# Kernel tuning notes

Measured on AMD Instinct MI355X. Metric: run time of the kernel, lower is better.

## Reference

```python
import jax, jax.numpy as jnp
import numpy as np

HIDDEN = 100


def gcn_conv(x, W, b, src, dst, w, n):
    # GCNConv with symmetric normalization (self-loops already appended).
    xw = x @ W                                   # [N, H]
    deg = jax.ops.segment_sum(w, dst, num_segments=n)
    dinv = jnp.where(deg > 0, jax.lax.rsqrt(deg), 0.0)
    norm = dinv[src] * w * dinv[dst]             # [E]
    agg = jax.ops.segment_sum(norm[:, None] * xw[src], dst, num_segments=n)
    return agg + b


def setup_inputs() -> dict:
    key = jax.random.key(0)
    ks = jax.random.split(key, 16)
    N, F, E, H = 100000, 128, 1600000, HIDDEN
    x = jax.random.normal(ks[0], (N, F), dtype=jnp.float32)
    edge_index = jax.random.randint(ks[1], (2, E), 0, N, dtype=jnp.int64)
    edge_weight = jax.random.uniform(ks[2], (E,), dtype=jnp.float32)
    sF = 1.0 / np.sqrt(F)
    sH2 = 1.0 / np.sqrt(2 * H)
    sH = 1.0 / np.sqrt(H)
    inp = {
        "x": x, "edge_index": edge_index, "edge_weight": edge_weight,
        "Wcz": jax.random.normal(ks[3], (F, H), jnp.float32) * sF,
        "bcz": jnp.zeros((H,), jnp.float32),
        "Wcr": jax.random.normal(ks[4], (F, H), jnp.float32) * sF,
        "bcr": jnp.zeros((H,), jnp.float32),
        "Wch": jax.random.normal(ks[5], (F, H), jnp.float32) * sF,
        "bch": jnp.zeros((H,), jnp.float32),
        "Wlz": jax.random.normal(ks[6], (2 * H, H), jnp.float32) * sH2,
        "blz": jnp.zeros((H,), jnp.float32),
        "Wlr": jax.random.normal(ks[7], (2 * H, H), jnp.float32) * sH2,
        "blr": jnp.zeros((H,), jnp.float32),
        "Wlh": jax.random.normal(ks[8], (2 * H, H), jnp.float32) * sH2,
        "blh": jnp.zeros((H,), jnp.float32),
        "Wout": jax.random.normal(ks[9], (H, 1), jnp.float32) * sH,
        "bout": jnp.zeros((1,), jnp.float32),
    }
    return inp


def reference(x, edge_index, edge_weight,
              Wcz, bcz, Wcr, bcr, Wch, bch,
              Wlz, blz, Wlr, blr, Wlh, blh,
              Wout, bout):
    N = x.shape[0]
    # add self-loops with weight 1 (GCNConv default)
    loop = jnp.arange(N, dtype=edge_index.dtype)
    src = jnp.concatenate([edge_index[0], loop])
    dst = jnp.concatenate([edge_index[1], loop])
    w = jnp.concatenate([edge_weight, jnp.ones((N,), edge_weight.dtype)])

    H0 = jnp.zeros((N, HIDDEN), x.dtype)  # TGCN initial hidden state

    cz = gcn_conv(x, Wcz, bcz, src, dst, w, N)
    Z = jax.nn.sigmoid(jnp.concatenate([cz, H0], axis=1) @ Wlz + blz)

    cr = gcn_conv(x, Wcr, bcr, src, dst, w, N)
    R = jax.nn.sigmoid(jnp.concatenate([cr, H0], axis=1) @ Wlr + blr)

    ch = gcn_conv(x, Wch, bch, src, dst, w, N)
    Ht = jnp.tanh(jnp.concatenate([ch, H0 * R], axis=1) @ Wlh + blh)

    Hn = Z * H0 + (1.0 - Z) * Ht
    h = jax.nn.relu(Hn)
    return h @ Wout + bout
```

## Files before the change

### kernel.cpp

```cpp
#include <hip/hip_runtime.h>

#define FEAT 128
#define HID  100
#define CHUNK 2048

typedef __attribute__((ext_vector_type(8))) short short8;
typedef __attribute__((ext_vector_type(4))) float f32x4;

__device__ __forceinline__ unsigned short f2bf(float f) {
    union { float f; unsigned int u; } v; v.f = f;
    unsigned int r = v.u + 0x7fffu + ((v.u >> 16) & 1u);
    return (unsigned short)(r >> 16);
}

__device__ __forceinline__ int get_edge(const void* ei, int f64, long long pos) {
    return f64 ? (int)((const long long*)ei)[pos] : ((const int*)ei)[pos];
}

__device__ __forceinline__ int detect_f64(const void* ei) {
    const int* p = (const int*)ei;
    unsigned long long b = __ballot(p[2 * (threadIdx.x & 63) + 1] == 0);
    return b == ~0ull;
}

__device__ __forceinline__ void scan_buckets(const int* __restrict__ bucketCnt,
                                             int NB, int* bs) {
    int t = threadIdx.x;
    int v = (t < NB) ? bucketCnt[t] : 0;
    if (t < NB) bs[t] = v;
    __syncthreads();
    for (int off = 1; off < NB; off <<= 1) {
        int tv = (t < NB && t >= off) ? bs[t - off] : 0;
        __syncthreads();
        if (t < NB) bs[t] += tv;
        __syncthreads();
    }
    int incl = (t < NB) ? bs[t] : 0;
    __syncthreads();
    if (t < NB) bs[t] = incl - v;
    if (t == NB - 1) bs[NB] = incl;
    __syncthreads();
}

__global__ __launch_bounds__(256)
void k_front(const float* __restrict__ Wcz, const float* __restrict__ bcz,
             const float* __restrict__ Wch, const float* __restrict__ bch,
             const float* __restrict__ Wlz, const float* __restrict__ blz,
             const float* __restrict__ Wlh, const float* __restrict__ blh,
             const float* __restrict__ Wout,
             unsigned short* __restrict__ WB, float* __restrict__ bfold_ext,
             float* __restrict__ WoutZ,
             const void* ei, int* __restrict__ bucketCnt,
             int* __restrict__ blockBase, int NB, int E) {
    const int FOLDB = 130;
    __shared__ int hist[1024];
    if (blockIdx.x < FOLDB) {
        int idx = blockIdx.x * 256 + threadIdx.x;
        if (idx < FEAT * 256) {
            int k = idx >> 8, n = idx & 255;
            float val = 0.f;
            if (n < HID) {
                for (int m = 0; m < HID; m++) val += Wcz[k * HID + m] * Wlz[m * HID + n];
            } else if (n >= 128 && n < 128 + HID) {
                int c = n - 128;
                for (int m = 0; m < HID; m++) val += Wch[k * HID + m] * Wlh[m * HID + c];
            }
            int ni = n >> 4, lc = n & 15, ks = k >> 5, hi = (k >> 3) & 3, j = k & 7;
            WB[(((ni * 4 + ks) * 64 + hi * 16 + lc) << 3) + j] = f2bf(val);
        } else if (idx < FEAT * 256 + 256) {
            int c = idx - FEAT * 256;
            float v = 0.f;
            if (c < HID) {
                v = blz[c];
                for (int j = 0; j < HID; j++) v += bcz[j] * Wlz[j * HID + c];
            } else if (c >= 128 && c < 128 + HID) {
                int cc = c - 128;
                v = blh[cc];
                for (int j = 0; j < HID; j++) v += bch[j] * Wlh[j * HID + cc];
            }
            bfold_ext[c] = v;
        } else if (idx < FEAT * 256 + 256 + 128) {
            int c = idx - FEAT * 256 - 256;
            WoutZ[c] = (c < HID) ? Wout[c] : 0.f;
        }
        return;
    }
    int f64 = detect_f64(ei);
    int cb = blockIdx.x - FOLDB;
    int t = threadIdx.x;
    for (int i = t; i < NB; i += 256) hist[i] = 0;
    __syncthreads();
    int e0 = cb * CHUNK;
#pragma unroll
    for (int k = 0; k < CHUNK / 256; k++) {
        int e = e0 + k * 256 + t;
        if (e < E) {
            int d = get_edge(ei, f64, (long long)E + e);
            atomicAdd(&hist[d >> 8], 1);
        }
    }
    __syncthreads();
    int* bb = blockBase + (size_t)cb * NB;
    for (int b = t; b < NB; b += 256) {
        int c = hist[b];
        if (c) bb[b] = atomicAdd(&bucketCnt[b], c);
    }
}

__global__ __launch_bounds__(512)
void k_scvt(const float* __restrict__ x, uint4* __restrict__ xb, int n8,
            const void* ei, const float* __restrict__ w,
            const int* __restrict__ bucketCnt, const int* __restrict__ blockBase,
            int2* __restrict__ sc, int NB, int E) {
    const int CVTB = 1024;
    __shared__ int hist[1024];
    __shared__ int bs[1024];
    if (blockIdx.x < CVTB) {
        int stride = CVTB * 512;
        for (int i = blockIdx.x * 512 + threadIdx.x; i < n8; i += stride) {
            float4 a = *(const float4*)(x + (size_t)i * 8);
            float4 b = *(const float4*)(x + (size_t)i * 8 + 4);
            uint4 o;
            o.x = f2bf(a.x) | ((unsigned)f2bf(a.y) << 16);
            o.y = f2bf(a.z) | ((unsigned)f2bf(a.w) << 16);
            o.z = f2bf(b.x) | ((unsigned)f2bf(b.y) << 16);
            o.w = f2bf(b.z) | ((unsigned)f2bf(b.w) << 16);
            xb[i] = o;
        }
        return;
    }
    int f64 = detect_f64(ei);
    int cb = blockIdx.x - CVTB;
    int t = threadIdx.x;
    scan_buckets(bucketCnt, NB, bs);
    for (int i = t; i < NB; i += 512) hist[i] = 0;
    __syncthreads();
    int e0 = cb * CHUNK;
    const int* bb = blockBase + (size_t)cb * NB;
    int sA[4], dA[4], wA[4], ok[4];
#pragma unroll
    for (int k = 0; k < 4; k++) {
        int e = e0 + k * 512 + t;
        ok[k] = (e < E);
        if (ok[k]) {
            sA[k] = get_edge(ei, f64, e);
            dA[k] = get_edge(ei, f64, (long long)E + e);
            wA[k] = __float_as_int(w[e]);
        }
    }
#pragma unroll
    for (int k = 0; k < 4; k++) {
        if (ok[k]) {
            int b = dA[k] >> 8;
            int r = atomicAdd(&hist[b], 1);
            int pos = bs[b] + bb[b] + r;
            long long val = ((long long)wA[k] << 32)
                          | (unsigned)(sA[k] | ((dA[k] & 255) << 24));
            *(long long*)&sc[pos] = val;
        }
    }
}

__global__ __launch_bounds__(512)
void k_bucket(const int2* __restrict__ sc, const int* __restrict__ bucketCnt,
              int* __restrict__ offs, int* __restrict__ cnt,
              int2* __restrict__ csr, float* __restrict__ dinv, int N, int NB) {
    __shared__ int bs[1024];
    __shared__ int hist[256];
    __shared__ int offsL[256];
    __shared__ int rank[256];
    __shared__ float wsum[256];
    int t = threadIdx.x;
    scan_buckets(bucketCnt, NB, bs);
    int n0 = blockIdx.x << 8;
    int s = bs[blockIdx.x], e = bs[blockIdx.x + 1];
    if (t < 256) { hist[t] = 0; rank[t] = 0; wsum[t] = 0.f; }
    __syncthreads();
    for (int i = s + t; i < e; i += 512)
        atomicAdd(&hist[((unsigned)sc[i].x) >> 24], 1);
    __syncthreads();
    int v = 0;
    if (t < 256) {
        v = (n0 + t < N) ? hist[t] + 1 : 0;
        offsL[t] = v;
    }
    __syncthreads();
    for (int off = 1; off < 256; off <<= 1) {
        int tv = (t < 256 && t >= off) ? offsL[t - off] : 0;
        __syncthreads();
        if (t < 256) offsL[t] += tv;
        __syncthreads();
    }
    int myOff = 0, myHist = 0;
    if (t < 256) { myOff = offsL[t] - v; myHist = hist[t]; }
    int csrBase = s + n0;
    if (t < 256 && n0 + t < N) {
        offs[n0 + t] = csrBase + myOff;
        cnt[n0 + t] = v;
    }
    __syncthreads();
    if (t < 256) offsL[t] = myOff;
    __syncthreads();
    for (int i = s + t; i < e; i += 512) {
        int2 en = sc[i];
        int dlow = ((unsigned)en.x) >> 24;
        int r = atomicAdd(&rank[dlow], 1);
        csr[csrBase + offsL[dlow] + r] = make_int2(en.x & 0xFFFFFF, en.y);
        atomicAdd(&wsum[dlow], __int_as_float(en.y));
    }
    __syncthreads();
    if (t < 256 && n0 + t < N) {
        dinv[n0 + t] = rsqrtf(1.f + wsum[t]);
        csr[csrBase + myOff + myHist] = make_int2(n0 + t, __float_as_int(1.0f));
    }
}

__global__ __launch_bounds__(256)
void k_agg4(const unsigned short* __restrict__ xb, const float* __restrict__ dinv,
            const int* __restrict__ offs, const int* __restrict__ cnt,
            const int2* __restrict__ csr, unsigned short* __restrict__ aggx, int N) {
    int wid  = __builtin_amdgcn_readfirstlane(threadIdx.x >> 6);
    int lane = threadIdx.x & 63;
    long long node = (long long)blockIdx.x * 4 + wid;
    if (node >= N) return;
    int q  = lane >> 3;
    int fl = lane & 7;
    float acc[16];
#pragma unroll
    for (int j = 0; j < 16; j++) acc[j] = 0.f;
    int rs = offs[node];
    int c  = cnt[node];
    for (int i = q; i < c; i += 8) {
        int2 e = csr[rs + i];
        float nr = __int_as_float(e.y) * dinv[e.x];
        const uint4* xp = (const uint4*)(xb + (size_t)e.x * FEAT + fl * 16);
        uint4 v0 = xp[0];
        uint4 v1 = xp[1];
        const unsigned* u0 = &v0.x;
        const unsigned* u1 = &v1.x;
#pragma unroll
        for (int j = 0; j < 4; j++) {
            acc[2*j]         += nr * __uint_as_float(u0[j] << 16);
            acc[2*j + 1]     += nr * __uint_as_float(u0[j] & 0xffff0000u);
            acc[8 + 2*j]     += nr * __uint_as_float(u1[j] << 16);
            acc[8 + 2*j + 1] += nr * __uint_as_float(u1[j] & 0xffff0000u);
        }
    }
#pragma unroll
    for (int j = 0; j < 16; j++) {
        acc[j] += __shfl_xor(acc[j], 8);
        acc[j] += __shfl_xor(acc[j], 16);
        acc[j] += __shfl_xor(acc[j], 32);
    }
    if (q == 0) {
        float dn = dinv[node];
        uint4 o0, o1;
        unsigned* p0 = &o0.x;
        unsigned* p1 = &o1.x;
#pragma unroll
        for (int j = 0; j < 4; j++) {
            p0[j] = f2bf(acc[2*j] * dn)   | ((unsigned)f2bf(acc[2*j+1] * dn) << 16);
            p1[j] = f2bf(acc[8+2*j] * dn) | ((unsigned)f2bf(acc[8+2*j+1] * dn) << 16);
        }
        uint4* op = (uint4*)(aggx + (size_t)node * FEAT + fl * 16);
        op[0] = o0;
        op[1] = o1;
    }
}

__global__ __launch_bounds__(256)
void k_post3(const unsigned short* __restrict__ aggx, const unsigned short* __restrict__ WB,
             const float* __restrict__ bfold_ext, const float* __restrict__ WoutZ,
             const float* __restrict__ bout, float* __restrict__ out, int N) {
    __shared__ unsigned short At[64 * 136];
    __shared__ float red[64 * 4];
    int t = threadIdx.x;
    int lane = t & 63;
    int w = __builtin_amdgcn_readfirstlane(t >> 6);
    long long base = (long long)blockIdx.x * 64;

    for (int it = 0; it < 4; it++) {
        int idx = it * 256 + t;
        int row = idx >> 4, c16 = idx & 15;
        long long grow = base + row;
        uint4 v = make_uint4(0u, 0u, 0u, 0u);
        if (grow < N) v = *(const uint4*)(aggx + grow * FEAT + c16 * 8);
        *(uint4*)(At + row * 136 + c16 * 8) = v;
    }
    __syncthreads();

    int l15 = lane & 15, lhi = lane >> 4;
    int tadd = 2 * w;
    f32x4 acc[4][4];
#pragma unroll
    for (int ti = 0; ti < 4; ti++)
#pragma unroll
        for (int mi = 0; mi < 4; mi++) acc[ti][mi] = (f32x4)0.f;

    const int tiles[4] = {tadd, tadd + 1, tadd + 8, tadd + 9};
#pragma unroll
    for (int ks = 0; ks < 4; ks++) {
        short8 a[4];
#pragma unroll
        for (int mi = 0; mi < 4; mi++)
            a[mi] = *(const short8*)(At + (mi * 16 + l15) * 136 + ks * 32 + lhi * 8);
        short8 b[4];
#pragma unroll
        for (int ti = 0; ti < 4; ti++)
            b[ti] = *(const short8*)(WB + (((tiles[ti] * 4 + ks) * 64 + lane) << 3));
#pragma unroll
        for (int ti = 0; ti < 4; ti++)
#pragma unroll
            for (int mi = 0; mi < 4; mi++)
                acc[ti][mi] = __builtin_amdgcn_mfma_f32_16x16x32_bf16(
                    a[mi], b[ti], acc[ti][mi], 0, 0, 0);
    }

    float partial[4][4];
#pragma unroll
    for (int mi = 0; mi < 4; mi++)
#pragma unroll
        for (int r = 0; r < 4; r++) partial[mi][r] = 0.f;
#pragma unroll
    for (int d = 0; d < 2; d++) {
        int zcol = (tadd + d) * 16 + l15;
        float bz = bfold_ext[zcol];
        float bh = bfold_ext[zcol + 128];
        float wo = WoutZ[zcol];
#pragma unroll
        for (int mi = 0; mi < 4; mi++)
#pragma unroll
            for (int r = 0; r < 4; r++) {
                float az = acc[d][mi][r] + bz;
                float ah = acc[d + 2][mi][r] + bh;
                float z  = 1.f / (1.f + expf(-az));
                float ht = tanhf(ah);
                float h  = (1.f - z) * ht;
                h = h > 0.f ? h : 0.f;
                partial[mi][r] += h * wo;
            }
    }
#pragma unroll
    for (int mi = 0; mi < 4; mi++)
#pragma unroll
        for (int r = 0; r < 4; r++) {
            float p = partial[mi][r];
            p += __shfl_xor(p, 1);
            p += __shfl_xor(p, 2);
            p += __shfl_xor(p, 4);
            p += __shfl_xor(p, 8);
            partial[mi][r] = p;
        }
    if (l15 == 0) {
#pragma unroll
        for (int mi = 0; mi < 4; mi++)
#pragma unroll
            for (int r = 0; r < 4; r++)
                red[(mi * 16 + lhi * 4 + r) * 4 + w] = partial[mi][r];
    }
    __syncthreads();
    if (t < 64) {
        long long node = base + t;
        if (node < N)
            out[node] = red[t * 4] + red[t * 4 + 1] + red[t * 4 + 2] + red[t * 4 + 3]
                      + bout[0];
    }
}

extern "C" void kernel_launch(void* const* d_in, const int* in_sizes, int n_in,
                              void* d_out, int out_size, void* d_ws, size_t ws_size,
                              hipStream_t stream) {
    const float* x    = (const float*)d_in[0];
    const void*  ei   = d_in[1];
    const float* ew   = (const float*)d_in[2];
    const float* Wcz  = (const float*)d_in[3];
    const float* bcz  = (const float*)d_in[4];
    const float* Wch  = (const float*)d_in[7];
    const float* bch  = (const float*)d_in[8];
    const float* Wlz  = (const float*)d_in[9];
    const float* blz  = (const float*)d_in[10];
    const float* Wlh  = (const float*)d_in[13];
    const float* blh  = (const float*)d_in[14];
    const float* Wout = (const float*)d_in[15];
    const float* bout = (const float*)d_in[16];
    float* out = (float*)d_out;

    int N = in_sizes[0] / FEAT;
    int E = in_sizes[2];
    int NB = (N + 255) >> 8;
    int nblocksA = (E + CHUNK - 1) / CHUNK;

    char* p = (char*)d_ws;
    auto alloc = [&](size_t bytes) -> char* {
        char* r = p;
        p += (bytes + 255) & ~(size_t)255;
        return r;
    };
    float*          dinv        = (float*)alloc((size_t)N * 4);
    int*            cnt         = (int*)  alloc((size_t)N * 4);
    int*            offs        = (int*)  alloc((size_t)N * 4);
    int*            bucketCnt   = (int*)  alloc((size_t)(NB + 1) * 4);
    int2*           csr         = (int2*) alloc((size_t)(E + N) * 8);
    unsigned short* xb          = (unsigned short*)alloc((size_t)N * FEAT * 2);
    unsigned short* aggx        = (unsigned short*)alloc((size_t)N * FEAT * 2);
    unsigned short* WB          = (unsigned short*)alloc((size_t)FEAT * 256 * 2);
    float*          bfold_ext   = (float*)alloc(256 * 4);
    float*          WoutZ       = (float*)alloc(128 * 4);
    int2* sc        = (int2*)aggx;
    int*  blockBase = (int*)((char*)aggx + (size_t)E * 8);

    hipMemsetAsync(bucketCnt, 0, (size_t)NB * 4, stream);
    k_front<<<130 + nblocksA, 256, 0, stream>>>(
        Wcz, bcz, Wch, bch, Wlz, blz, Wlh, blh, Wout, WB, bfold_ext, WoutZ,
        ei, bucketCnt, blockBase, NB, E);
    k_scvt<<<1024 + nblocksA, 512, 0, stream>>>(
        x, (uint4*)xb, N * FEAT / 8, ei, ew, bucketCnt, blockBase, sc, NB, E);
    k_bucket<<<NB, 512, 0, stream>>>(sc, bucketCnt, offs, cnt, csr, dinv, N, NB);
    k_agg4<<<(N + 3) / 4, 256, 0, stream>>>(xb, dinv, offs, cnt, csr, aggx, N);
    k_post3<<<(N + 63) / 64, 256, 0, stream>>>(aggx, WB, bfold_ext, WoutZ, bout, out, N);
}
```

Measured before the change: 284.9 us.

## Fuse neighbor aggregation into the post GEMM kernel via shared memory tile

Merges the aggregation kernel and the post-processing GEMM kernel. Each block now aggregates its 64 nodes directly into the shared-memory A tile, so the bf16 aggregated feature matrix is never written to or re-read from global memory. The edge loop is also unrolled by two so each lane has two gathers in flight. In exchange, each wave processes 16 nodes serially with 1563 blocks instead of 25000, which lowers parallelism and may worsen load imbalance on skewed degrees. Scratch buffers for the sort are given their own allocation.

Measured after the change: 360.7 us. 1.27x slower.

```diff
diff --git a/kernel.cpp b/kernel.cpp
--- a/kernel.cpp
+++ b/kernel.cpp
@@ -216,76 +216,90 @@
 }
 
 __global__ __launch_bounds__(256)
-void k_agg4(const unsigned short* __restrict__ xb, const float* __restrict__ dinv,
-            const int* __restrict__ offs, const int* __restrict__ cnt,
-            const int2* __restrict__ csr, unsigned short* __restrict__ aggx, int N) {
-    int wid  = __builtin_amdgcn_readfirstlane(threadIdx.x >> 6);
-    int lane = threadIdx.x & 63;
-    long long node = (long long)blockIdx.x * 4 + wid;
-    if (node >= N) return;
-    int q  = lane >> 3;
-    int fl = lane & 7;
-    float acc[16];
-#pragma unroll
-    for (int j = 0; j < 16; j++) acc[j] = 0.f;
-    int rs = offs[node];
-    int c  = cnt[node];
-    for (int i = q; i < c; i += 8) {
-        int2 e = csr[rs + i];
-        float nr = __int_as_float(e.y) * dinv[e.x];
-        const uint4* xp = (const uint4*)(xb + (size_t)e.x * FEAT + fl * 16);
-        uint4 v0 = xp[0];
-        uint4 v1 = xp[1];
-        const unsigned* u0 = &v0.x;
-        const unsigned* u1 = &v1.x;
-#pragma unroll
-        for (int j = 0; j < 4; j++) {
-            acc[2*j]         += nr * __uint_as_float(u0[j] << 16);
-            acc[2*j + 1]     += nr * __uint_as_float(u0[j] & 0xffff0000u);
-            acc[8 + 2*j]     += nr * __uint_as_float(u1[j] << 16);
-            acc[8 + 2*j + 1] += nr * __uint_as_float(u1[j] & 0xffff0000u);
-        }
-    }
-#pragma unroll
-    for (int j = 0; j < 16; j++) {
-        acc[j] += __shfl_xor(acc[j], 8);
-        acc[j] += __shfl_xor(acc[j], 16);
-        acc[j] += __shfl_xor(acc[j], 32);
-    }
-    if (q == 0) {
-        float dn = dinv[node];
-        uint4 o0, o1;
-        unsigned* p0 = &o0.x;
-        unsigned* p1 = &o1.x;
-#pragma unroll
-        for (int j = 0; j < 4; j++) {
-            p0[j] = f2bf(acc[2*j] * dn)   | ((unsigned)f2bf(acc[2*j+1] * dn) << 16);
-            p1[j] = f2bf(acc[8+2*j] * dn) | ((unsigned)f2bf(acc[8+2*j+1] * dn) << 16);
-        }
-        uint4* op = (uint4*)(aggx + (size_t)node * FEAT + fl * 16);
-        op[0] = o0;
-        op[1] = o1;
-    }
-}
-
-__global__ __launch_bounds__(256)
-void k_post3(const unsigned short* __restrict__ aggx, const unsigned short* __restrict__ WB,
-             const float* __restrict__ bfold_ext, const float* __restrict__ WoutZ,
-             const float* __restrict__ bout, float* __restrict__ out, int N) {
+void k_aggpost(const unsigned short* __restrict__ xb, const float* __restrict__ dinv,
+               const int* __restrict__ offs, const int* __restrict__ cnt,
+               const int2* __restrict__ csr, const unsigned short* __restrict__ WB,
+               const float* __restrict__ bfold_ext, const float* __restrict__ WoutZ,
+               const float* __restrict__ bout, float* __restrict__ out, int N) {
     __shared__ unsigned short At[64 * 136];
     __shared__ float red[64 * 4];
     int t = threadIdx.x;
     int lane = t & 63;
     int w = __builtin_amdgcn_readfirstlane(t >> 6);
     long long base = (long long)blockIdx.x * 64;
-
-    for (int it = 0; it < 4; it++) {
-        int idx = it * 256 + t;
-        int row = idx >> 4, c16 = idx & 15;
-        long long grow = base + row;
-        uint4 v = make_uint4(0u, 0u, 0u, 0u);
-        if (grow < N) v = *(const uint4*)(aggx + grow * FEAT + c16 * 8);
-        *(uint4*)(At + row * 136 + c16 * 8) = v;
+    int q  = lane >> 3;
+    int fl = lane & 7;
+
+    for (int i = 0; i < 16; i++) {
+        long long node = base + w * 16 + i;
+        int row = w * 16 + i;
+        float acc[16];
+#pragma unroll
+        for (int j = 0; j < 16; j++) acc[j] = 0.f;
+        if (node < N) {
+            int rs = offs[node];
+            int c  = cnt[node];
+            int ii = q;
+            for (; ii + 8 < c; ii += 16) {
+                int2 e0 = csr[rs + ii];
+                int2 e1 = csr[rs + ii + 8];
+                float nr0 = __int_as_float(e0.y) * dinv[e0.x];
+                float nr1 = __int_as_float(e1.y) * dinv[e1.x];
+                const uint4* xp0 = (const uint4*)(xb + (size_t)e0.x * FEAT + fl * 16);
+                const uint4* xp1 = (const uint4*)(xb + (size_t)e1.x * FEAT + fl * 16);
+                uint4 a0 = xp0[0], a1 = xp0[1];
+                uint4 b0 = xp1[0], b1 = xp1[1];
+                const unsigned* ua0 = &a0.x;
+                const unsigned* ua1 = &a1.x;
+                const unsigned* ub0 = &b0.x;
+                const unsigned* ub1 = &b1.x;
+#pragma unroll
+                for (int j = 0; j < 4; j++) {
+                    acc[2*j]         += nr0 * __uint_as_float(ua0[j] << 16);
+                    acc[2*j + 1]     += nr0 * __uint_as_float(ua0[j] & 0xffff0000u);
+                    acc[8 + 2*j]     += nr0 * __uint_as_float(ua1[j] << 16);
+                    acc[8 + 2*j + 1] += nr0 * __uint_as_float(ua1[j] & 0xffff0000u);
+                    acc[2*j]         += nr1 * __uint_as_float(ub0[j] << 16);
+                    acc[2*j + 1]     += nr1 * __uint_as_float(ub0[j] & 0xffff0000u);
+                    acc[8 + 2*j]     += nr1 * __uint_as_float(ub1[j] << 16);
+                    acc[8 + 2*j + 1] += nr1 * __uint_as_float(ub1[j] & 0xffff0000u);
+                }
+            }
+            if (ii < c) {
+                int2 e0 = csr[rs + ii];
+                float nr0 = __int_as_float(e0.y) * dinv[e0.x];
+                const uint4* xp0 = (const uint4*)(xb + (size_t)e0.x * FEAT + fl * 16);
+                uint4 a0 = xp0[0], a1 = xp0[1];
+                const unsigned* ua0 = &a0.x;
+                const unsigned* ua1 = &a1.x;
+#pragma unroll
+                for (int j = 0; j < 4; j++) {
+                    acc[2*j]         += nr0 * __uint_as_float(ua0[j] << 16);
+                    acc[2*j + 1]     += nr0 * __uint_as_float(ua0[j] & 0xffff0000u);
+                    acc[8 + 2*j]     += nr0 * __uint_as_float(ua1[j] << 16);
+                    acc[8 + 2*j + 1] += nr0 * __uint_as_float(ua1[j] & 0xffff0000u);
+                }
+            }
+        }
+#pragma unroll
+        for (int j = 0; j < 16; j++) {
+            acc[j] += __shfl_xor(acc[j], 8);
+            acc[j] += __shfl_xor(acc[j], 16);
+            acc[j] += __shfl_xor(acc[j], 32);
+        }
+        if (q == 0) {
+            float dn = (node < N) ? dinv[node] : 0.f;
+            uint4 o0, o1;
+            unsigned* p0 = &o0.x;
+            unsigned* p1 = &o1.x;
+#pragma unroll
+            for (int j = 0; j < 4; j++) {
+                p0[j] = f2bf(acc[2*j] * dn)   | ((unsigned)f2bf(acc[2*j+1] * dn) << 16);
+                p1[j] = f2bf(acc[8+2*j] * dn) | ((unsigned)f2bf(acc[8+2*j+1] * dn) << 16);
+            }
+            *(uint4*)(At + row * 136 + fl * 16)     = o0;
+            *(uint4*)(At + row * 136 + fl * 16 + 8) = o1;
+        }
     }
     __syncthreads();
 
@@ -402,12 +416,12 @@
     int*            bucketCnt   = (int*)  alloc((size_t)(NB + 1) * 4);
     int2*           csr         = (int2*) alloc((size_t)(E + N) * 8);
     unsigned short* xb          = (unsigned short*)alloc((size_t)N * FEAT * 2);
-    unsigned short* aggx        = (unsigned short*)alloc((size_t)N * FEAT * 2);
+    char*           scratch     = alloc((size_t)E * 8 + (size_t)nblocksA * NB * 4 + 256);
     unsigned short* WB          = (unsigned short*)alloc((size_t)FEAT * 256 * 2);
     float*          bfold_ext   = (float*)alloc(256 * 4);
     float*          WoutZ       = (float*)alloc(128 * 4);
-    int2* sc        = (int2*)aggx;
-    int*  blockBase = (int*)((char*)aggx + (size_t)E * 8);
+    int2* sc        = (int2*)scratch;
+    int*  blockBase = (int*)(scratch + (size_t)E * 8);
 
     hipMemsetAsync(bucketCnt, 0, (size_t)NB * 4, stream);
     k_front<<<130 + nblocksA, 256, 0, stream>>>(
@@ -416,6 +430,6 @@
     k_scvt<<<1024 + nblocksA, 512, 0, stream>>>(
         x, (uint4*)xb, N * FEAT / 8, ei, ew, bucketCnt, blockBase, sc, NB, E);
     k_bucket<<<NB, 512, 0, stream>>>(sc, bucketCnt, offs, cnt, csr, dinv, N, NB);
-    k_agg4<<<(N + 3) / 4, 256, 0, stream>>>(xb, dinv, offs, cnt, csr, aggx, N);
-    k_post3<<<(N + 63) / 64, 256, 0, stream>>>(aggx, WB, bfold_ext, WoutZ, bout, out, N);
-}
+    k_aggpost<<<(N + 63) / 64, 256, 0, stream>>>(
+        xb, dinv, offs, cnt, csr, WB, bfold_ext, WoutZ, bout, out, N);
+}
```
